# Performance work log

Hardware: AMD Instinct MI355X
Metric: run time of the kernel (lower is better)

## Reference

```python
import jax, jax.numpy as jnp
import numpy as np

SEQ, BATCH, HIDDEN = 2048, 1, 4096
NUM_HEADS, NUM_KV_HEADS, HEAD_DIM = 32, 8, 128
Q_PER_GROUP = NUM_HEADS // NUM_KV_HEADS  # 4
TOTAL_PROJ = NUM_KV_HEADS * (Q_PER_GROUP + 2) * HEAD_DIM  # 6144


def setup_inputs() -> dict:
    key = jax.random.key(0)
    k1, k2, k3 = jax.random.split(key, 3)
    tokens = jax.random.normal(k1, (SEQ, BATCH, HIDDEN), dtype=jnp.float32)
    # xavier-ish scaling so activations stay sane
    weight_qkv = jax.random.normal(k2, (TOTAL_PROJ, HIDDEN), dtype=jnp.float32) * (2.0 / (TOTAL_PROJ + HIDDEN)) ** 0.5
    weight_proj = jax.random.normal(k3, (HIDDEN, NUM_HEADS * HEAD_DIM), dtype=jnp.float32) * (2.0 / (HIDDEN + NUM_HEADS * HEAD_DIM)) ** 0.5
    return {"tokens": tokens, "weight_qkv": weight_qkv, "weight_proj": weight_proj}


def reference(tokens, weight_qkv, weight_proj):
    S, B, H = tokens.shape
    scale = 1.0 / HEAD_DIM ** 0.5
    # QKV projection with interleaved GQA layout: per KV group [q0..q_{g-1}, k, v]
    qkv = jnp.einsum('sbh,ph->sbp', tokens, weight_qkv)
    qkv = qkv.reshape(S, B, NUM_KV_HEADS, Q_PER_GROUP + 2, HEAD_DIM)
    q = qkv[:, :, :, :Q_PER_GROUP, :].reshape(S, B, NUM_HEADS, HEAD_DIM)
    k = qkv[:, :, :, Q_PER_GROUP, :]       # [S,B,KVH,D]
    v = qkv[:, :, :, Q_PER_GROUP + 1, :]
    # repeat_interleave KV heads to match Q heads (GQA)
    k = jnp.repeat(k, Q_PER_GROUP, axis=2)
    v = jnp.repeat(v, Q_PER_GROUP, axis=2)
    # [S,B,H,D] -> [B,H,S,D]
    q = q.transpose(1, 2, 0, 3)
    k = k.transpose(1, 2, 0, 3)
    v = v.transpose(1, 2, 0, 3)
    scores = jnp.einsum('bhsd,bhtd->bhst', q, k) * scale
    causal = jnp.tril(jnp.ones((S, S), dtype=bool))
    scores = jnp.where(causal, scores, jnp.finfo(scores.dtype).min)
    attn = jax.nn.softmax(scores, axis=-1)
    out = jnp.einsum('bhst,bhtd->bhsd', attn, v)
    # [B,H,S,D] -> [S,B,H*D]
    out = out.transpose(2, 0, 1, 3).reshape(S, B, NUM_HEADS * HEAD_DIM)
    return jnp.einsum('sbe,he->sbh', out, weight_proj)
```

## Files before the change

### kernel.cpp

```cpp
#include <hip/hip_runtime.h>
#include <hip/hip_bf16.h>
#include <stdint.h>

#define SEQ 2048
#define HIDDEN 4096
#define NHEADS 32
#define HD 128
#define QKV_LD 6144
#define OUT_LD 4096

typedef __attribute__((ext_vector_type(8))) short short8;
typedef __attribute__((ext_vector_type(4))) short short4v;
typedef __attribute__((ext_vector_type(4))) float f32x4;
typedef __attribute__((ext_vector_type(4))) int int4v;
typedef __attribute__((ext_vector_type(2))) unsigned int uint2v;
typedef __attribute__((ext_vector_type(4))) float float4v;

__device__ __forceinline__ short f2bf(float f) {
  uint32_t u = __builtin_bit_cast(uint32_t, f);
  u += 0x7fff + ((u >> 16) & 1);
  return (short)(u >> 16);
}

__global__ void cast_kernel(const float* __restrict__ in, short* __restrict__ out, int n4) {
  int stride = gridDim.x * blockDim.x;
  for (int i = blockIdx.x * blockDim.x + threadIdx.x; i < n4; i += stride) {
    float4v v = ((const float4v*)in)[i];
    short4v o;
    o[0] = f2bf(v[0]); o[1] = f2bf(v[1]); o[2] = f2bf(v[2]); o[3] = f2bf(v[3]);
    ((short4v*)out)[i] = o;
  }
}

template <typename OT>
__global__ __launch_bounds__(512, 2) void gemm256(const short* __restrict__ A,
                                                  const short* __restrict__ B,
                                                  OT* __restrict__ C,
                                                  int M, int N, int K, int NT) {
  __shared__ __align__(16) short lds[65536];
  const int tid = threadIdx.x;
  const int w = tid >> 6, lane = tid & 63;
  const int wr = w >> 2, wc = w & 3;
  const int llo = lane & 15, lhi = lane >> 4;

  const int nwg = gridDim.x;
  const int cpx = nwg >> 3;
  const int work = ((int)blockIdx.x & 7) * cpx + ((int)blockIdx.x >> 3);
  const int mt = work / NT, nt = work % NT;
  const size_t arow0 = (size_t)mt * 256, brow0 = (size_t)nt * 256;
  const short* Ab = A + arow0 * K;
  const short* Bb = B + brow0 * K;

  const int s_r = lane >> 3;
  const int s_c = lane & 7;

  const int NKT = K >> 6;
  const int NIT = NKT >> 1;

  f32x4 acc[8][4] = {};
  short8 af[4][2], bf[4][2];

  auto STAGE = [&](int kt, int h) {
    const int bufd = kt & 1;
    const int side = h >> 1;
    const int htrow = (h & 1) << 7;
    const short* gb = side ? Bb : Ab;
#pragma unroll
    for (int c = 0; c < 2; c++) {
      const int slice = (c << 3) + w;
      const int rowrel = htrow + (slice << 3) + s_r;
      const short* src = gb + (size_t)rowrel * K + (kt << 6) + ((s_c ^ (rowrel & 7)) << 3);
      short* dst = lds + (side << 15) + (bufd << 14) + htrow * 64 + (slice << 9);
      __builtin_amdgcn_global_load_lds(
          (const __attribute__((address_space(1))) uint32_t*)src,
          (__attribute__((address_space(3))) uint32_t*)dst, 16, 0, 0);
    }
  };

  auto LDA = [&](int bufd, int m, int kk) -> short8 {
    const int row = (wr << 7) + (m << 4) + llo;
    const int ch = ((kk << 2) + lhi) ^ (row & 7);
    return *(const short8*)(lds + (bufd << 14) + row * 64 + (ch << 3));
  };
  auto LDB = [&](int bufd, int n, int kk) -> short8 {
    const int row = (wc << 6) + (n << 4) + llo;
    const int ch = ((kk << 2) + lhi) ^ (row & 7);
    return *(const short8*)(lds + 32768 + (bufd << 14) + row * 64 + (ch << 3));
  };
  auto QUAD = [&](int mh, int nh) {
    __builtin_amdgcn_s_setprio(1);
#pragma unroll
    for (int mi = 0; mi < 4; mi++)
#pragma unroll
      for (int ni = 0; ni < 2; ni++)
#pragma unroll
        for (int kk = 0; kk < 2; kk++)
          acc[(mh << 2) + mi][(nh << 1) + ni] = __builtin_amdgcn_mfma_f32_16x16x32_bf16(
              af[mi][kk], bf[(nh << 1) + ni][kk], acc[(mh << 2) + mi][(nh << 1) + ni], 0, 0, 0);
    __builtin_amdgcn_s_setprio(0);
  };

  STAGE(0, 0); STAGE(0, 1); STAGE(0, 2); STAGE(0, 3);
  STAGE(1, 0); STAGE(1, 1);
  asm volatile("s_waitcnt vmcnt(4)" ::: "memory");
  __builtin_amdgcn_s_barrier();

  for (int it = 0; it < NIT; ++it) {
    const int T1 = 2 * it + 1;
    const bool stN = (it + 1 < NIT);
#pragma unroll
    for (int mi = 0; mi < 4; mi++) { af[mi][0] = LDA(0, mi, 0); af[mi][1] = LDA(0, mi, 1); }
#pragma unroll
    for (int ni = 0; ni < 2; ni++) { bf[ni][0] = LDB(0, ni, 0); bf[ni][1] = LDB(0, ni, 1); }
    STAGE(T1, 2); STAGE(T1, 3);
    __builtin_amdgcn_s_barrier();
    asm volatile("s_waitcnt lgkmcnt(0)" ::: "memory");
    __builtin_amdgcn_sched_barrier(0);
    QUAD(0, 0);
    __builtin_amdgcn_s_barrier();
#pragma unroll
    for (int ni = 0; ni < 2; ni++) { bf[2 + ni][0] = LDB(0, 2 + ni, 0); bf[2 + ni][1] = LDB(0, 2 + ni, 1); }
    __builtin_amdgcn_s_barrier();
    asm volatile("s_waitcnt lgkmcnt(0)" ::: "memory");
    __builtin_amdgcn_sched_barrier(0);
    QUAD(0, 1);
    __builtin_amdgcn_s_barrier();
#pragma unroll
    for (int mi = 0; mi < 4; mi++) { af[mi][0] = LDA(0, 4 + mi, 0); af[mi][1] = LDA(0, 4 + mi, 1); }
    __builtin_amdgcn_s_barrier();
    asm volatile("s_waitcnt lgkmcnt(0)" ::: "memory");
    __builtin_amdgcn_sched_barrier(0);
    QUAD(1, 0);
    __builtin_amdgcn_s_barrier();
    if (stN) { STAGE(T1 + 1, 0); STAGE(T1 + 1, 1); }
    __builtin_amdgcn_s_barrier();
    __builtin_amdgcn_sched_barrier(0);
    QUAD(1, 1);
    if (stN) asm volatile("s_waitcnt vmcnt(4)" ::: "memory");
    else     asm volatile("s_waitcnt vmcnt(0)" ::: "memory");
    __builtin_amdgcn_s_barrier();
#pragma unroll
    for (int mi = 0; mi < 4; mi++) { af[mi][0] = LDA(1, mi, 0); af[mi][1] = LDA(1, mi, 1); }
#pragma unroll
    for (int ni = 0; ni < 2; ni++) { bf[ni][0] = LDB(1, ni, 0); bf[ni][1] = LDB(1, ni, 1); }
    if (stN) { STAGE(T1 + 1, 2); STAGE(T1 + 1, 3); }
    __builtin_amdgcn_s_barrier();
    asm volatile("s_waitcnt lgkmcnt(0)" ::: "memory");
    __builtin_amdgcn_sched_barrier(0);
    QUAD(0, 0);
    __builtin_amdgcn_s_barrier();
#pragma unroll
    for (int ni = 0; ni < 2; ni++) { bf[2 + ni][0] = LDB(1, 2 + ni, 0); bf[2 + ni][1] = LDB(1, 2 + ni, 1); }
    __builtin_amdgcn_s_barrier();
    asm volatile("s_waitcnt lgkmcnt(0)" ::: "memory");
    __builtin_amdgcn_sched_barrier(0);
    QUAD(0, 1);
    __builtin_amdgcn_s_barrier();
#pragma unroll
    for (int mi = 0; mi < 4; mi++) { af[mi][0] = LDA(1, 4 + mi, 0); af[mi][1] = LDA(1, 4 + mi, 1); }
    __builtin_amdgcn_s_barrier();
    asm volatile("s_waitcnt lgkmcnt(0)" ::: "memory");
    __builtin_amdgcn_sched_barrier(0);
    QUAD(1, 0);
    __builtin_amdgcn_s_barrier();
    if (stN) { STAGE(T1 + 2, 0); STAGE(T1 + 2, 1); }
    __builtin_amdgcn_s_barrier();
    __builtin_amdgcn_sched_barrier(0);
    QUAD(1, 1);
    if (stN) asm volatile("s_waitcnt vmcnt(4)" ::: "memory");
    __builtin_amdgcn_s_barrier();
  }

#pragma unroll
  for (int m = 0; m < 8; m++)
#pragma unroll
    for (int n = 0; n < 4; n++)
#pragma unroll
      for (int r = 0; r < 4; r++) {
        const size_t row = arow0 + (wr << 7) + (m << 4) + (lhi << 2) + r;
        const size_t col = brow0 + (wc << 6) + (n << 4) + llo;
        const float v = acc[m][n][r];
        if constexpr (sizeof(OT) == 2) C[row * N + col] = f2bf(v);
        else                           C[row * N + col] = v;
      }
}

template <typename OT>
__global__ __launch_bounds__(256) void gemm_bt(const short* __restrict__ A,
                                               const short* __restrict__ B,
                                               OT* __restrict__ C,
                                               int M, int N, int K) {
  __shared__ __align__(16) short As[128 * 32];
  __shared__ __align__(16) short Bs[128 * 32];
  const int tid = threadIdx.x;
  const int wave = tid >> 6, lane = tid & 63;
  const int lhi = lane >> 4, llo = lane & 15;
  const int wm = wave >> 1, wn = wave & 1;
  const size_t arow0 = (size_t)blockIdx.x * 128;
  const size_t brow0 = (size_t)blockIdx.y * 128;
  const int srow = lane >> 2, schunk = lane & 3;

  f32x4 acc[4][4] = {};

  const short* aB = A + arow0 * K;
  const short* bB = B + brow0 * K;

  for (int k0 = 0; k0 < K; k0 += 32) {
    __syncthreads();
#pragma unroll
    for (int c = 0; c < 2; c++) {
      const int call = wave + c * 4;
      const int row = call * 16 + srow;
      __builtin_amdgcn_global_load_lds(
          (const __attribute__((address_space(1))) uint32_t*)(aB + (size_t)row * K + k0 + schunk * 8),
          (__attribute__((address_space(3))) uint32_t*)(As + call * 512), 16, 0, 0);
      __builtin_amdgcn_global_load_lds(
          (const __attribute__((address_space(1))) uint32_t*)(bB + (size_t)row * K + k0 + schunk * 8),
          (__attribute__((address_space(3))) uint32_t*)(Bs + call * 512), 16, 0, 0);
    }
    __syncthreads();

    short8 af[4], bf[4];
#pragma unroll
    for (int i = 0; i < 4; i++) {
      af[i] = *(const short8*)(As + (wm * 64 + i * 16 + llo) * 32 + lhi * 8);
      bf[i] = *(const short8*)(Bs + (wn * 64 + i * 16 + llo) * 32 + lhi * 8);
    }
#pragma unroll
    for (int i = 0; i < 4; i++)
#pragma unroll
      for (int j = 0; j < 4; j++)
        acc[i][j] = __builtin_amdgcn_mfma_f32_16x16x32_bf16(af[i], bf[j], acc[i][j], 0, 0, 0);
  }

#pragma unroll
  for (int i = 0; i < 4; i++)
#pragma unroll
    for (int j = 0; j < 4; j++)
#pragma unroll
      for (int r = 0; r < 4; r++) {
        size_t row = arow0 + wm * 64 + i * 16 + lhi * 4 + r;
        size_t col = brow0 + wn * 64 + j * 16 + llo;
        float v = acc[i][j][r];
        if constexpr (sizeof(OT) == 2) C[row * N + col] = f2bf(v);
        else                           C[row * N + col] = v;
      }
}

__global__ __launch_bounds__(256, 2) void attn_fwd(const short* __restrict__ qkv,
                                                   short* __restrict__ aout) {
  const int qt = gridDim.y - 1 - blockIdx.y;
  const int h = blockIdx.x;
  const int kvh = h >> 2, g = h & 3;
  const int tid = threadIdx.x;
  const int wave = tid >> 6, lane = tid & 63;
  const int lhi = lane >> 4, llo = lane & 15;

  __shared__ __align__(16) short Ksm[2][64 * 128];
  __shared__ __align__(16) short Vsm[2][64 * 128];
  __shared__ __align__(16) short Psm[4][16 * 72];

  const float scale = 0.08838834764831845f;

  const int qrow = qt * 64 + wave * 16 + llo;
  const short* qbase = qkv + (size_t)qrow * QKV_LD + (kvh * 6 + g) * HD;
  short8 qf[4];
#pragma unroll
  for (int kk = 0; kk < 4; kk++) qf[kk] = *(const short8*)(qbase + kk * 32 + lhi * 8);

  f32x4 o[8] = {};
  float mrow[4], lrow[4];
#pragma unroll
  for (int r = 0; r < 4; r++) { mrow[r] = -1e30f; lrow[r] = 0.f; }

  const short* Kg = qkv + (kvh * 6 + 4) * HD;
  const short* Vg = qkv + (kvh * 6 + 5) * HD;

  const int k_row = lhi;
  const int v_vr = tid >> 4, v_vc = tid & 15;

  auto STAGE_K = [&](int t, int buf) {
#pragma unroll
    for (int c = 0; c < 4; c++) {
      const int call = wave * 4 + c;
      const int row = call * 4 + k_row;
      const int sc = llo ^ (row & 7);
      __builtin_amdgcn_global_load_lds(
          (const __attribute__((address_space(1))) uint32_t*)(Kg + (size_t)(t * 64 + row) * QKV_LD + sc * 8),
          (__attribute__((address_space(3))) uint32_t*)(&Ksm[buf][0] + call * 512), 16, 0, 0);
    }
  };
  short8 vreg[4];
  auto LOAD_V = [&](int t) {
#pragma unroll
    for (int c = 0; c < 4; c++) {
      const int vr = c * 16 + v_vr;
      vreg[c] = *(const short8*)(Vg + (size_t)(t * 64 + vr) * QKV_LD + v_vc * 8);
    }
  };
  auto WRITE_V = [&](int buf) {
#pragma unroll
    for (int c = 0; c < 4; c++) {
      const int vr = c * 16 + v_vr;
      *(short8*)(&Vsm[buf][0] + ((vr >> 2) * 8 + (v_vc >> 1)) * 64 + (vr & 3) * 16 + (v_vc & 1) * 8) = vreg[c];
    }
  };

  const uint32_t vlane0 = (uint32_t)(uintptr_t)(__attribute__((address_space(3))) short*)(&Vsm[0][0])
                          + (uint32_t)(lhi * 2048 + llo * 8);

  STAGE_K(0, 0);
  LOAD_V(0);
  asm volatile("s_waitcnt vmcnt(0)" ::: "memory");
  WRITE_V(0);
  __syncthreads();

  const int ntiles = qt + 1;
  for (int t = 0; t < ntiles; t++) {
    const int cur = t & 1, nxt = cur ^ 1;
    const bool pf = (t + 1 < ntiles);
    if (pf) { STAGE_K(t + 1, nxt); LOAD_V(t + 1); }

    const short* Kc = &Ksm[cur][0];
    f32x4 s[4] = {};
#pragma unroll
    for (int n = 0; n < 4; n++) {
#pragma unroll
      for (int kk = 0; kk < 4; kk++) {
        const int krow = n * 16 + llo;
        const int ch = (kk * 4 + lhi) ^ (krow & 7);
        short8 kf = *(const short8*)(Kc + krow * 128 + ch * 8);
        s[n] = __builtin_amdgcn_mfma_f32_16x16x32_bf16(qf[kk], kf, s[n], 0, 0, 0);
      }
    }

    float sv[4][4];
    const bool diag = (t == qt);
#pragma unroll
    for (int n = 0; n < 4; n++)
#pragma unroll
      for (int r = 0; r < 4; r++) {
        float x = s[n][r] * scale;
        if (diag && (n * 16 + llo > wave * 16 + lhi * 4 + r)) x = -1e30f;
        sv[n][r] = x;
      }

    float rm4[4];
#pragma unroll
    for (int r = 0; r < 4; r++) {
      float rm = fmaxf(fmaxf(sv[0][r], sv[1][r]), fmaxf(sv[2][r], sv[3][r]));
#pragma unroll
      for (int msk = 1; msk < 16; msk <<= 1) rm = fmaxf(rm, __shfl_xor(rm, msk));
      rm4[r] = rm;
    }
    bool need = false;
#pragma unroll
    for (int r = 0; r < 4; r++) need = need || (rm4[r] > mrow[r] + 8.0f);
    if (__any(need)) {
#pragma unroll
      for (int r = 0; r < 4; r++) {
        const float mnew = fmaxf(mrow[r], rm4[r]);
        const float a = __expf(mrow[r] - mnew);
        mrow[r] = mnew;
        lrow[r] *= a;
#pragma unroll
        for (int nn = 0; nn < 8; nn++) o[nn][r] *= a;
      }
    }
#pragma unroll
    for (int r = 0; r < 4; r++) {
      float rs = 0.f;
#pragma unroll
      for (int n = 0; n < 4; n++) {
        float p = __expf(sv[n][r] - mrow[r]);
        sv[n][r] = p;
        rs += p;
      }
#pragma unroll
      for (int msk = 1; msk < 16; msk <<= 1) rs += __shfl_xor(rs, msk);
      lrow[r] += rs;
    }

    short* P = &Psm[wave][0];
#pragma unroll
    for (int n = 0; n < 4; n++)
#pragma unroll
      for (int r = 0; r < 4; r++)
        P[(lhi * 4 + r) * 72 + n * 16 + llo] = f2bf(sv[n][r]);

    short8 pa0 = *(const short8*)(P + llo * 72 + lhi * 8);
    short8 pa1 = *(const short8*)(P + llo * 72 + 32 + lhi * 8);
    const uint32_t vlane = vlane0 + (uint32_t)(cur * 16384);
#pragma unroll
    for (int ks = 0; ks < 2; ks++) {
      uint2v vr_[8][2];
#pragma unroll
      for (int nn = 0; nn < 8; nn++)
#pragma unroll
        for (int hh = 0; hh < 2; hh++) {
          uint32_t a = vlane + (uint32_t)(ks * 8192 + hh * 1024 + nn * 128);
          asm volatile("ds_read_b64_tr_b16 %0, %1" : "=v"(vr_[nn][hh]) : "v"(a));
        }
      asm volatile("s_waitcnt lgkmcnt(0)" ::: "memory");
      __builtin_amdgcn_sched_barrier(0);
      const short8 pa = ks ? pa1 : pa0;
#pragma unroll
      for (int nn = 0; nn < 8; nn++) {
        int4v tv;
        tv[0] = (int)vr_[nn][0][0]; tv[1] = (int)vr_[nn][0][1];
        tv[2] = (int)vr_[nn][1][0]; tv[3] = (int)vr_[nn][1][1];
        o[nn] = __builtin_amdgcn_mfma_f32_16x16x32_bf16(pa, __builtin_bit_cast(short8, tv), o[nn], 0, 0, 0);
      }
    }

    if (pf) {
      asm volatile("s_waitcnt vmcnt(0)" ::: "memory");
      __syncthreads();
      WRITE_V(nxt);
      __syncthreads();
    }
  }

#pragma unroll
  for (int nn = 0; nn < 8; nn++)
#pragma unroll
    for (int r = 0; r < 4; r++) {
      const size_t row = qt * 64 + wave * 16 + lhi * 4 + r;
      const size_t col = (size_t)h * HD + nn * 16 + llo;
      aout[row * OUT_LD + col] = f2bf(o[nn][r] / lrow[r]);
    }
}

extern "C" void kernel_launch(void* const* d_in, const int* in_sizes, int n_in,
                              void* d_out, int out_size, void* d_ws, size_t ws_size,
                              hipStream_t stream) {
  const float* tokens = (const float*)d_in[0];
  const float* wqkv   = (const float*)d_in[1];
  const float* wproj  = (const float*)d_in[2];
  float* out = (float*)d_out;

  short* tok_bf   = (short*)d_ws;
  short* wqkv_bf  = tok_bf   + (size_t)SEQ * HIDDEN;
  short* wproj_bf = wqkv_bf  + (size_t)QKV_LD * HIDDEN;
  short* qkv_bf   = wproj_bf + (size_t)HIDDEN * OUT_LD;
  short* attn_bf  = qkv_bf   + (size_t)SEQ * QKV_LD;

  cast_kernel<<<2048, 256, 0, stream>>>(tokens, tok_bf, SEQ * HIDDEN / 4);
  cast_kernel<<<2048, 256, 0, stream>>>(wqkv, wqkv_bf, QKV_LD * HIDDEN / 4);
  cast_kernel<<<2048, 256, 0, stream>>>(wproj, wproj_bf, HIDDEN * OUT_LD / 4);

  gemm256<short><<<192, 512, 0, stream>>>(tok_bf, wqkv_bf, qkv_bf, SEQ, QKV_LD, HIDDEN, QKV_LD / 256);

  attn_fwd<<<dim3(NHEADS, SEQ / 64), 256, 0, stream>>>(qkv_bf, attn_bf);

  gemm_bt<float><<<dim3(SEQ / 128, OUT_LD / 128), 256, 0, stream>>>(
      attn_bf, wproj_bf, out, SEQ, OUT_LD, HIDDEN);
}
```

Measured before the change: 373.9 us.

## Generalize 256-row GEMM to variable N-tile and use it for both projections

Templates the 256-row GEMM on the N tile width (64*NBF), so the QKV projection uses 256x192 tiles (256 blocks, which fits 256 CUs better than 192 blocks) and the output projection uses 256x128 tiles in place of the simple single-buffered 128x128 gemm_bt. The k-loop is restructured into HALF steps that load the full B fragment once and stream A fragments in pairs. Each k-tile is staged whole and waited on with adjusted vmcnt counts. The aim is better CU occupancy and more data reuse, with some risk from the changed register pressure and load/compute interleaving.

```diff
diff --git a/kernel.cpp b/kernel.cpp
--- a/kernel.cpp
+++ b/kernel.cpp
@@ -32,12 +32,12 @@
   }
 }
 
-template <typename OT>
-__global__ __launch_bounds__(512, 2) void gemm256(const short* __restrict__ A,
-                                                  const short* __restrict__ B,
-                                                  OT* __restrict__ C,
-                                                  int M, int N, int K, int NT) {
-  __shared__ __align__(16) short lds[65536];
+template <typename OT, int NBF>
+__global__ __launch_bounds__(512, 2) void gemm256b(const short* __restrict__ A,
+                                                   const short* __restrict__ B,
+                                                   OT* __restrict__ C,
+                                                   int M, int N, int K, int NT) {
+  __shared__ __align__(16) short lds[32768 + NBF * 8192];
   const int tid = threadIdx.x;
   const int w = tid >> 6, lane = tid & 63;
   const int wr = w >> 2, wc = w & 3;
@@ -47,34 +47,37 @@
   const int cpx = nwg >> 3;
   const int work = ((int)blockIdx.x & 7) * cpx + ((int)blockIdx.x >> 3);
   const int mt = work / NT, nt = work % NT;
-  const size_t arow0 = (size_t)mt * 256, brow0 = (size_t)nt * 256;
+  const size_t arow0 = (size_t)mt * 256, brow0 = (size_t)nt * (NBF * 64);
   const short* Ab = A + arow0 * K;
   const short* Bb = B + brow0 * K;
 
-  const int s_r = lane >> 3;
-  const int s_c = lane & 7;
-
-  const int NKT = K >> 6;
-  const int NIT = NKT >> 1;
-
-  f32x4 acc[8][4] = {};
-  short8 af[4][2], bf[4][2];
-
-  auto STAGE = [&](int kt, int h) {
+  f32x4 acc[8][NBF] = {};
+
+  auto STAGE_A = [&](int kt, int j) {
     const int bufd = kt & 1;
-    const int side = h >> 1;
-    const int htrow = (h & 1) << 7;
-    const short* gb = side ? Bb : Ab;
-#pragma unroll
-    for (int c = 0; c < 2; c++) {
-      const int slice = (c << 3) + w;
-      const int rowrel = htrow + (slice << 3) + s_r;
-      const short* src = gb + (size_t)rowrel * K + (kt << 6) + ((s_c ^ (rowrel & 7)) << 3);
-      short* dst = lds + (side << 15) + (bufd << 14) + htrow * 64 + (slice << 9);
-      __builtin_amdgcn_global_load_lds(
-          (const __attribute__((address_space(1))) uint32_t*)src,
-          (__attribute__((address_space(3))) uint32_t*)dst, 16, 0, 0);
-    }
+    const int r0 = (j << 6) + (w << 3);
+    const int row = r0 + (lane >> 3);
+    const short* src = Ab + (size_t)row * K + (kt << 6) + (((lane & 7) ^ (row & 7)) << 3);
+    short* dst = lds + (bufd << 14) + r0 * 64;
+    __builtin_amdgcn_global_load_lds(
+        (const __attribute__((address_space(1))) uint32_t*)src,
+        (__attribute__((address_space(3))) uint32_t*)dst, 16, 0, 0);
+  };
+  auto STAGE_B = [&](int kt, int j) {
+    const int bufd = kt & 1;
+    const int r0 = (j << 6) + (w << 3);
+    const int row = r0 + (lane >> 3);
+    const short* src = Bb + (size_t)row * K + (kt << 6) + (((lane & 7) ^ (row & 7)) << 3);
+    short* dst = lds + 32768 + bufd * (NBF << 12) + r0 * 64;
+    __builtin_amdgcn_global_load_lds(
+        (const __attribute__((address_space(1))) uint32_t*)src,
+        (__attribute__((address_space(3))) uint32_t*)dst, 16, 0, 0);
+  };
+  auto STAGE = [&](int kt) {
+#pragma unroll
+    for (int j = 0; j < 4; j++) STAGE_A(kt, j);
+#pragma unroll
+    for (int j = 0; j < NBF; j++) STAGE_B(kt, j);
   };
 
   auto LDA = [&](int bufd, int m, int kk) -> short8 {
@@ -83,165 +86,106 @@
     return *(const short8*)(lds + (bufd << 14) + row * 64 + (ch << 3));
   };
   auto LDB = [&](int bufd, int n, int kk) -> short8 {
-    const int row = (wc << 6) + (n << 4) + llo;
+    const int row = wc * (NBF << 4) + (n << 4) + llo;
     const int ch = ((kk << 2) + lhi) ^ (row & 7);
-    return *(const short8*)(lds + 32768 + (bufd << 14) + row * 64 + (ch << 3));
-  };
-  auto QUAD = [&](int mh, int nh) {
-    __builtin_amdgcn_s_setprio(1);
-#pragma unroll
-    for (int mi = 0; mi < 4; mi++)
-#pragma unroll
-      for (int ni = 0; ni < 2; ni++)
-#pragma unroll
-        for (int kk = 0; kk < 2; kk++)
-          acc[(mh << 2) + mi][(nh << 1) + ni] = __builtin_amdgcn_mfma_f32_16x16x32_bf16(
-              af[mi][kk], bf[(nh << 1) + ni][kk], acc[(mh << 2) + mi][(nh << 1) + ni], 0, 0, 0);
-    __builtin_amdgcn_s_setprio(0);
-  };
-
-  STAGE(0, 0); STAGE(0, 1); STAGE(0, 2); STAGE(0, 3);
-  STAGE(1, 0); STAGE(1, 1);
-  asm volatile("s_waitcnt vmcnt(4)" ::: "memory");
-  __builtin_amdgcn_s_barrier();
-
-  for (int it = 0; it < NIT; ++it) {
-    const int T1 = 2 * it + 1;
-    const bool stN = (it + 1 < NIT);
-#pragma unroll
-    for (int mi = 0; mi < 4; mi++) { af[mi][0] = LDA(0, mi, 0); af[mi][1] = LDA(0, mi, 1); }
-#pragma unroll
-    for (int ni = 0; ni < 2; ni++) { bf[ni][0] = LDB(0, ni, 0); bf[ni][1] = LDB(0, ni, 1); }
-    STAGE(T1, 2); STAGE(T1, 3);
+    return *(const short8*)(lds + 32768 + bufd * (NBF << 12) + row * 64 + (ch << 3));
+  };
+
+  auto HALF = [&](int bufd, int ktStage, bool doStage, bool gateFinal) {
+    short8 b_[NBF][2], a_[2][2], an_[2][2], an2_[2][2];
+#pragma unroll
+    for (int n = 0; n < NBF; n++) { b_[n][0] = LDB(bufd, n, 0); b_[n][1] = LDB(bufd, n, 1); }
+#pragma unroll
+    for (int mi = 0; mi < 2; mi++) { a_[mi][0] = LDA(bufd, mi, 0); a_[mi][1] = LDA(bufd, mi, 1); }
     __builtin_amdgcn_s_barrier();
     asm volatile("s_waitcnt lgkmcnt(0)" ::: "memory");
     __builtin_amdgcn_sched_barrier(0);
-    QUAD(0, 0);
-    __builtin_amdgcn_s_barrier();
-#pragma unroll
-    for (int ni = 0; ni < 2; ni++) { bf[2 + ni][0] = LDB(0, 2 + ni, 0); bf[2 + ni][1] = LDB(0, 2 + ni, 1); }
+    __builtin_amdgcn_s_setprio(1);
+#pragma unroll
+    for (int mi = 0; mi < 2; mi++)
+#pragma unroll
+      for (int n = 0; n < NBF; n++)
+#pragma unroll
+        for (int kk = 0; kk < 2; kk++)
+          acc[mi][n] = __builtin_amdgcn_mfma_f32_16x16x32_bf16(a_[mi][kk], b_[n][kk], acc[mi][n], 0, 0, 0);
+    __builtin_amdgcn_s_setprio(0);
+    __builtin_amdgcn_s_barrier();
+#pragma unroll
+    for (int mi = 0; mi < 2; mi++) {
+      an_[mi][0] = LDA(bufd, 2 + mi, 0);  an_[mi][1] = LDA(bufd, 2 + mi, 1);
+      an2_[mi][0] = LDA(bufd, 4 + mi, 0); an2_[mi][1] = LDA(bufd, 4 + mi, 1);
+    }
     __builtin_amdgcn_s_barrier();
     asm volatile("s_waitcnt lgkmcnt(0)" ::: "memory");
     __builtin_amdgcn_sched_barrier(0);
-    QUAD(0, 1);
-    __builtin_amdgcn_s_barrier();
-#pragma unroll
-    for (int mi = 0; mi < 4; mi++) { af[mi][0] = LDA(0, 4 + mi, 0); af[mi][1] = LDA(0, 4 + mi, 1); }
+    __builtin_amdgcn_s_setprio(1);
+#pragma unroll
+    for (int mi = 0; mi < 2; mi++)
+#pragma unroll
+      for (int n = 0; n < NBF; n++)
+#pragma unroll
+        for (int kk = 0; kk < 2; kk++)
+          acc[2 + mi][n] = __builtin_amdgcn_mfma_f32_16x16x32_bf16(an_[mi][kk], b_[n][kk], acc[2 + mi][n], 0, 0, 0);
+    __builtin_amdgcn_s_setprio(0);
+    __builtin_amdgcn_s_barrier();
+#pragma unroll
+    for (int mi = 0; mi < 2; mi++) { a_[mi][0] = LDA(bufd, 6 + mi, 0); a_[mi][1] = LDA(bufd, 6 + mi, 1); }
     __builtin_amdgcn_s_barrier();
     asm volatile("s_waitcnt lgkmcnt(0)" ::: "memory");
     __builtin_amdgcn_sched_barrier(0);
-    QUAD(1, 0);
-    __builtin_amdgcn_s_barrier();
-    if (stN) { STAGE(T1 + 1, 0); STAGE(T1 + 1, 1); }
+    __builtin_amdgcn_s_setprio(1);
+#pragma unroll
+    for (int mi = 0; mi < 2; mi++)
+#pragma unroll
+      for (int n = 0; n < NBF; n++)
+#pragma unroll
+        for (int kk = 0; kk < 2; kk++)
+          acc[4 + mi][n] = __builtin_amdgcn_mfma_f32_16x16x32_bf16(an2_[mi][kk], b_[n][kk], acc[4 + mi][n], 0, 0, 0);
+    __builtin_amdgcn_s_setprio(0);
+    __builtin_amdgcn_s_barrier();
+    if (doStage) STAGE(ktStage);
     __builtin_amdgcn_s_barrier();
     __builtin_amdgcn_sched_barrier(0);
-    QUAD(1, 1);
-    if (stN) asm volatile("s_waitcnt vmcnt(4)" ::: "memory");
-    else     asm volatile("s_waitcnt vmcnt(0)" ::: "memory");
-    __builtin_amdgcn_s_barrier();
-#pragma unroll
-    for (int mi = 0; mi < 4; mi++) { af[mi][0] = LDA(1, mi, 0); af[mi][1] = LDA(1, mi, 1); }
-#pragma unroll
-    for (int ni = 0; ni < 2; ni++) { bf[ni][0] = LDB(1, ni, 0); bf[ni][1] = LDB(1, ni, 1); }
-    if (stN) { STAGE(T1 + 1, 2); STAGE(T1 + 1, 3); }
-    __builtin_amdgcn_s_barrier();
-    asm volatile("s_waitcnt lgkmcnt(0)" ::: "memory");
-    __builtin_amdgcn_sched_barrier(0);
-    QUAD(0, 0);
-    __builtin_amdgcn_s_barrier();
-#pragma unroll
-    for (int ni = 0; ni < 2; ni++) { bf[2 + ni][0] = LDB(1, 2 + ni, 0); bf[2 + ni][1] = LDB(1, 2 + ni, 1); }
-    __builtin_amdgcn_s_barrier();
-    asm volatile("s_waitcnt lgkmcnt(0)" ::: "memory");
-    __builtin_amdgcn_sched_barrier(0);
-    QUAD(0, 1);
-    __builtin_amdgcn_s_barrier();
-#pragma unroll
-    for (int mi = 0; mi < 4; mi++) { af[mi][0] = LDA(1, 4 + mi, 0); af[mi][1] = LDA(1, 4 + mi, 1); }
-    __builtin_amdgcn_s_barrier();
-    asm volatile("s_waitcnt lgkmcnt(0)" ::: "memory");
-    __builtin_amdgcn_sched_barrier(0);
-    QUAD(1, 0);
-    __builtin_amdgcn_s_barrier();
-    if (stN) { STAGE(T1 + 2, 0); STAGE(T1 + 2, 1); }
-    __builtin_amdgcn_s_barrier();
-    __builtin_amdgcn_sched_barrier(0);
-    QUAD(1, 1);
-    if (stN) asm volatile("s_waitcnt vmcnt(4)" ::: "memory");
-    __builtin_amdgcn_s_barrier();
+    __builtin_amdgcn_s_setprio(1);
+#pragma unroll
+    for (int mi = 0; mi < 2; mi++)
+#pragma unroll
+      for (int n = 0; n < NBF; n++)
+#pragma unroll
+        for (int kk = 0; kk < 2; kk++)
+          acc[6 + mi][n] = __builtin_amdgcn_mfma_f32_16x16x32_bf16(a_[mi][kk], b_[n][kk], acc[6 + mi][n], 0, 0, 0);
+    __builtin_amdgcn_s_setprio(0);
+    if (doStage) {
+      if constexpr (NBF == 3) asm volatile("s_waitcnt vmcnt(7)" ::: "memory");
+      else                    asm volatile("s_waitcnt vmcnt(6)" ::: "memory");
+    } else if (gateFinal) {
+      asm volatile("s_waitcnt vmcnt(0)" ::: "memory");
+    }
+    __builtin_amdgcn_s_barrier();
+  };
+
+  STAGE(0);
+  STAGE(1);
+  if constexpr (NBF == 3) asm volatile("s_waitcnt vmcnt(7)" ::: "memory");
+  else                    asm volatile("s_waitcnt vmcnt(6)" ::: "memory");
+  __builtin_amdgcn_s_barrier();
+
+  const int NIT = (K >> 6) >> 1;
+  for (int it = 0; it < NIT; ++it) {
+    const bool stN = (it + 1 < NIT);
+    HALF(0, 2 * it + 2, stN, !stN);
+    HALF(1, 2 * it + 3, stN, false);
   }
 
 #pragma unroll
   for (int m = 0; m < 8; m++)
 #pragma unroll
-    for (int n = 0; n < 4; n++)
+    for (int n = 0; n < NBF; n++)
 #pragma unroll
       for (int r = 0; r < 4; r++) {
         const size_t row = arow0 + (wr << 7) + (m << 4) + (lhi << 2) + r;
-        const size_t col = brow0 + (wc << 6) + (n << 4) + llo;
+        const size_t col = brow0 + wc * (NBF << 4) + (n << 4) + llo;
         const float v = acc[m][n][r];
-        if constexpr (sizeof(OT) == 2) C[row * N + col] = f2bf(v);
-        else                           C[row * N + col] = v;
-      }
-}
-
-template <typename OT>
-__global__ __launch_bounds__(256) void gemm_bt(const short* __restrict__ A,
-                                               const short* __restrict__ B,
-                                               OT* __restrict__ C,
-                                               int M, int N, int K) {
-  __shared__ __align__(16) short As[128 * 32];
-  __shared__ __align__(16) short Bs[128 * 32];
-  const int tid = threadIdx.x;
-  const int wave = tid >> 6, lane = tid & 63;
-  const int lhi = lane >> 4, llo = lane & 15;
-  const int wm = wave >> 1, wn = wave & 1;
-  const size_t arow0 = (size_t)blockIdx.x * 128;
-  const size_t brow0 = (size_t)blockIdx.y * 128;
-  const int srow = lane >> 2, schunk = lane & 3;
-
-  f32x4 acc[4][4] = {};
-
-  const short* aB = A + arow0 * K;
-  const short* bB = B + brow0 * K;
-
-  for (int k0 = 0; k0 < K; k0 += 32) {
-    __syncthreads();
-#pragma unroll
-    for (int c = 0; c < 2; c++) {
-      const int call = wave + c * 4;
-      const int row = call * 16 + srow;
-      __builtin_amdgcn_global_load_lds(
-          (const __attribute__((address_space(1))) uint32_t*)(aB + (size_t)row * K + k0 + schunk * 8),
-          (__attribute__((address_space(3))) uint32_t*)(As + call * 512), 16, 0, 0);
-      __builtin_amdgcn_global_load_lds(
-          (const __attribute__((address_space(1))) uint32_t*)(bB + (size_t)row * K + k0 + schunk * 8),
-          (__attribute__((address_space(3))) uint32_t*)(Bs + call * 512), 16, 0, 0);
-    }
-    __syncthreads();
-
-    short8 af[4], bf[4];
-#pragma unroll
-    for (int i = 0; i < 4; i++) {
-      af[i] = *(const short8*)(As + (wm * 64 + i * 16 + llo) * 32 + lhi * 8);
-      bf[i] = *(const short8*)(Bs + (wn * 64 + i * 16 + llo) * 32 + lhi * 8);
-    }
-#pragma unroll
-    for (int i = 0; i < 4; i++)
-#pragma unroll
-      for (int j = 0; j < 4; j++)
-        acc[i][j] = __builtin_amdgcn_mfma_f32_16x16x32_bf16(af[i], bf[j], acc[i][j], 0, 0, 0);
-  }
-
-#pragma unroll
-  for (int i = 0; i < 4; i++)
-#pragma unroll
-    for (int j = 0; j < 4; j++)
-#pragma unroll
-      for (int r = 0; r < 4; r++) {
-        size_t row = arow0 + wm * 64 + i * 16 + lhi * 4 + r;
-        size_t col = brow0 + wn * 64 + j * 16 + llo;
-        float v = acc[i][j][r];
         if constexpr (sizeof(OT) == 2) C[row * N + col] = f2bf(v);
         else                           C[row * N + col] = v;
       }
@@ -449,10 +393,9 @@
   cast_kernel<<<2048, 256, 0, stream>>>(wqkv, wqkv_bf, QKV_LD * HIDDEN / 4);
   cast_kernel<<<2048, 256, 0, stream>>>(wproj, wproj_bf, HIDDEN * OUT_LD / 4);
 
-  gemm256<short><<<192, 512, 0, stream>>>(tok_bf, wqkv_bf, qkv_bf, SEQ, QKV_LD, HIDDEN, QKV_LD / 256);
+  gemm256b<short, 3><<<256, 512, 0, stream>>>(tok_bf, wqkv_bf, qkv_bf, SEQ, QKV_LD, HIDDEN, QKV_LD / 192);
 
   attn_fwd<<<dim3(NHEADS, SEQ / 64), 256, 0, stream>>>(qkv_bf, attn_bf);
 
-  gemm_bt<float><<<dim3(SEQ / 128, OUT_LD / 128), 256, 0, stream>>>(
-      attn_bf, wproj_bf, out, SEQ, OUT_LD, HIDDEN);
+  gemm256b<float, 2><<<256, 512, 0, stream>>>(attn_bf, wproj_bf, out, SEQ, OUT_LD, HIDDEN, OUT_LD / 128);
 }
```

Result: faster. 338.9 us (-9.4%).
